# Optimization experiments

Measured on AMD Instinct MI355X. Metric: run time of the kernel, lower is better.

The kernel has to match this reference:

```python
import jax, jax.numpy as jnp
import numpy as np
import math

EPS = 1e-5
GN_GROUPS = 32


def conv2d(x, w, padding):
    # x: [B,C,H,W], w: [O,I,kh,kw]
    return jax.lax.conv_general_dilated(
        x, w, window_strides=(1, 1), padding=[(padding, padding)] * 2,
        dimension_numbers=("NCHW", "OIHW", "NCHW"))


def group_norm(x, weight, bias, groups=GN_GROUPS, eps=EPS):
    B, C, H, W = x.shape
    xg = x.reshape(B, groups, C // groups, H, W)
    mu = xg.mean(axis=(2, 3, 4), keepdims=True)
    var = xg.var(axis=(2, 3, 4), keepdims=True)
    xn = (xg - mu) * jax.lax.rsqrt(var + eps)
    xn = xn.reshape(B, C, H, W)
    return xn * weight[None, :, None, None] + bias[None, :, None, None]


def setup_inputs() -> dict:
    key = jax.random.key(0)
    ks = jax.random.split(key, 8)
    B, C, H, W = 8, 256, 80, 80
    init_gate = 0.99
    gate_bias_val = 0.5 * math.log((1 + init_gate) / (1 - init_gate))
    return {
        "x": jax.random.normal(ks[0], (B, C, H, W), dtype=jnp.float32),
        "w1": jax.random.normal(ks[1], (C, C, 3, 3), dtype=jnp.float32) * 0.01,
        "gn1_w": jnp.ones((C,), dtype=jnp.float32),
        "gn1_b": jnp.zeros((C,), dtype=jnp.float32),
        "w2": jax.random.normal(ks[2], (C, C, 3, 3), dtype=jnp.float32) * 0.01,
        "gn2_w": jnp.ones((C,), dtype=jnp.float32),
        "gn2_b": jnp.zeros((C,), dtype=jnp.float32),
        "gate_w": jax.random.normal(ks[3], (1, C, 1, 1), dtype=jnp.float32) * 0.01,
        "gate_b": jnp.full((1,), gate_bias_val, dtype=jnp.float32),
    }


def reference(x, w1, gn1_w, gn1_b, w2, gn2_w, gn2_b, gate_w, gate_b):
    # shortcut is identity (in_channels == out_channels, stride 1)
    shortcut = x
    # conv1 -> GN -> ReLU
    h = jax.nn.relu(group_norm(conv2d(x, w1, padding=1), gn1_w, gn1_b))
    # conv2 -> GN
    h = group_norm(conv2d(h, w2, padding=1), gn2_w, gn2_b)
    # SpatialGate: 1x1 conv on the original input, ReTanH activation
    g = conv2d(x, gate_w, padding=0) + gate_b[None, :, None, None]  # [B,1,H,W]
    gate = jnp.clip(jnp.tanh(g), 0.0, None)
    # num_groups == 1: encode/decode are identity reshapes; gate broadcasts over C
    out = h * gate
    return jax.nn.relu(out + shortcut)
```

## Files before the change

### kernel.cpp

```cpp
#include <hip/hip_runtime.h>
#include <math.h>

#define NB   8
#define NC   256
#define NH   80
#define NW   80
#define NHW  6400
#define GN_EPS 1e-5f

typedef __bf16 bf16;
typedef bf16 bf16x2 __attribute__((ext_vector_type(2)));
typedef bf16 bf16x4 __attribute__((ext_vector_type(4)));
typedef bf16 bf16x8 __attribute__((ext_vector_type(8)));
typedef float f32x4 __attribute__((ext_vector_type(4)));

typedef __attribute__((address_space(1))) void gvoid;
typedef __attribute__((address_space(3))) void lvoid;
__device__ __forceinline__ void glds16(const void* g, void* l) {
    __builtin_amdgcn_global_load_lds((const gvoid*)g, (lvoid*)l, 16, 0, 0);
}

#define AW_Q 520
#define AW_T 2080
#define AW_BUF 18720

__global__ __launch_bounds__(256) void setup_kernel(
    const float* __restrict__ w1, const float* __restrict__ w2,
    bf16* __restrict__ wA1, bf16* __restrict__ wA2,
    float* __restrict__ stats)
{
    int blk = blockIdx.x, tid = threadIdx.x;
    if (blk == 0) {
        #pragma unroll
        for (int k = 0; k < 8; k++) stats[tid + k * 256] = 0.0f;
        return;
    }
    int rb = blk - 1;
    const float* w = (rb < 2304) ? w1 : w2;
    bf16* wA       = (rb < 2304) ? wA1 : wA2;
    int idx = (rb % 2304) * 256 + tid;
    int c8 = idx & 7;
    int co = (idx >> 3) & 255;
    int qq = (idx >> 11) & 3;
    int tc = idx >> 13;
    int tap = tc % 9, chunk = tc / 9;
    int ci = chunk * 32 + qq * 8 + c8;
    wA[idx] = (bf16)w[(size_t)(co * 256 + ci) * 9 + tap];
}

__global__ __launch_bounds__(256) void prep1_kernel(
    const float* __restrict__ x, bf16* __restrict__ xp,
    const float* __restrict__ gw, float* __restrict__ gpart)
{
    __shared__ float tile[8 * 84];
    int bid = blockIdx.x;
    int row = bid % 80;
    int cib = (bid / 80) & 31;
    int b   = bid / 2560;
    for (int e = threadIdx.x; e < 640; e += 256) {
        int c8 = e / 80, col = e - c8 * 80;
        tile[c8 * 84 + col] = x[((size_t)(b * NC + cib * 8 + c8) * NH + row) * NW + col];
    }
    __syncthreads();
    size_t base = (((size_t)(b * 32 + cib) * 82 + row + 1) * 82) * 8 + 8;
    for (int t = threadIdx.x; t < 320; t += 256) {
        int e = 2 * t, col = e >> 3, c8 = e & 7;
        bf16x2 pk = { (bf16)tile[c8 * 84 + col], (bf16)tile[(c8 + 1) * 84 + col] };
        *(bf16x2*)(xp + base + e) = pk;
    }
    if (threadIdx.x < 80) {
        int col = threadIdx.x;
        float s = 0.0f;
        #pragma unroll
        for (int c8 = 0; c8 < 8; c8++) s = fmaf(tile[c8 * 84 + col], gw[cib * 8 + c8], s);
        gpart[((size_t)cib * NB + b) * NHW + row * 80 + col] = s;
    }
    const uint4 z4 = make_uint4(0u, 0u, 0u, 0u);
    size_t img = ((size_t)(b * 32 + cib)) * 82;
    if (threadIdx.x < 2) {
        int col = threadIdx.x * 81;
        *(uint4*)(xp + ((img + row + 1) * 82 + col) * 8) = z4;
    }
    if (row == 0 || row == 79) {
        int prow = (row == 0) ? 0 : 81;
        for (int u = threadIdx.x; u < 82; u += 256)
            *(uint4*)(xp + ((img + prow) * 82 + u) * 8) = z4;
    }
}

__global__ __launch_bounds__(320, 3) void conv_kernel(
    const bf16* __restrict__ xp, const bf16* __restrict__ wA,
    bf16* __restrict__ y, float* __restrict__ ssum, float* __restrict__ ssq)
{
    __shared__ __align__(16) bf16 Aw[2 * AW_BUF];
    __shared__ float wgs[8], wgq[8];

    int tid  = threadIdx.x;
    int wid  = tid >> 6;
    int lane = tid & 63;
    int n = lane & 15, q = lane >> 4;

    int bid = blockIdx.x;
    int b   = bid >> 6;
    int rem = bid & 63;
    int ct  = rem >> 4;
    int rt  = rem & 15;
    int co0 = ct * 64, h0 = rt * 5;

    if (tid < 8) { wgs[tid] = 0.0f; wgq[tid] = 0.0f; }

    f32x4 acc[4][5];
    #pragma unroll
    for (int i = 0; i < 4; i++)
        #pragma unroll
        for (int j = 0; j < 5; j++) acc[i][j] = (f32x4){0.f, 0.f, 0.f, 0.f};

    for (int p = wid; p < 36; p += 5) {
        int tap = p >> 2, qq = p & 3;
        glds16((const char*)(wA + ((size_t)p * 256 + co0) * 8) + lane * 16,
               (char*)(Aw + tap * AW_T + qq * AW_Q) + lane * 16);
    }

    for (int c = 0; c < 8; c++) {
        __syncthreads();
        if (c + 1 < 8) {
            bf16* dst = Aw + (((c + 1) & 1) ? AW_BUF : 0);
            for (int p = wid; p < 36; p += 5) {
                int tap = p >> 2, qq = p & 3;
                glds16((const char*)(wA + ((size_t)((c + 1) * 36 + p) * 256 + co0) * 8) + lane * 16,
                       (char*)(dst + tap * AW_T + qq * AW_Q) + lane * 16);
            }
        }
        const bf16* awc = Aw + ((c & 1) ? AW_BUF : 0) + q * AW_Q + n * 8;
        const bf16* xq = xp + (((size_t)(b * 32 + c * 4 + q) * 82 + (h0 + wid)) * 82) * 8 + n * 8;

        #pragma unroll
        for (int r = 0; r < 3; r++) {
            bf16x8 L[15];
            #pragma unroll
            for (int nt = 0; nt < 5; nt++)
                #pragma unroll
                for (int s = 0; s < 3; s++)
                    L[nt * 3 + s] = *(const bf16x8*)(xq + (r * 82 + s + nt * 16) * 8);
            #pragma unroll
            for (int s = 0; s < 3; s++) {
                bf16x8 af[4];
                #pragma unroll
                for (int mt = 0; mt < 4; mt++)
                    af[mt] = *(const bf16x8*)(awc + (r * 3 + s) * AW_T + mt * 128);
                #pragma unroll
                for (int mt = 0; mt < 4; mt++)
                    #pragma unroll
                    for (int nt = 0; nt < 5; nt++)
                        acc[mt][nt] = __builtin_amdgcn_mfma_f32_16x16x32_bf16(
                            af[mt], L[nt * 3 + s], acc[mt][nt], 0, 0, 0);
            }
        }
    }

    int h = h0 + wid;
    #pragma unroll
    for (int mt = 0; mt < 4; mt++) {
        float s1 = 0.0f, s2 = 0.0f;
        int co  = co0 + mt * 16 + q * 4;
        int cib = co >> 3, c8 = co & 7;
        #pragma unroll
        for (int nt = 0; nt < 5; nt++) {
            int col = nt * 16 + n;
            bf16x4 pk;
            #pragma unroll
            for (int rg = 0; rg < 4; rg++) {
                float v = acc[mt][nt][rg];
                pk[rg] = (bf16)v;
                s1 += v;
                s2 = fmaf(v, v, s2);
            }
            *(bf16x4*)(y + ((((size_t)(b * 32 + cib) * 80 + h) * 80 + col) * 8 + c8)) = pk;
        }
        #pragma unroll
        for (int off = 1; off < 16; off <<= 1) {
            s1 += __shfl_xor(s1, off, 64);
            s2 += __shfl_xor(s2, off, 64);
        }
        if (n == 0) {
            int gl = mt * 2 + (q >> 1);
            atomicAdd(&wgs[gl], s1);
            atomicAdd(&wgq[gl], s2);
        }
    }
    __syncthreads();
    if (tid < 8) {
        atomicAdd(&ssum[b * 32 + ct * 8 + tid], wgs[tid]);
        atomicAdd(&ssq [b * 32 + ct * 8 + tid], wgq[tid]);
    }
}

__global__ __launch_bounds__(256) void prep2_kernel(
    const bf16* __restrict__ y, bf16* __restrict__ xp,
    const float* __restrict__ s, const float* __restrict__ sq,
    const float* __restrict__ gamma, const float* __restrict__ beta,
    const float* __restrict__ gpart, const float* __restrict__ gb,
    float* __restrict__ gate)
{
    int bid = blockIdx.x;
    if (bid >= 5120) {
        int i = (bid - 5120) * 256 + threadIdx.x;
        float gs = gb[0];
        #pragma unroll 8
        for (int k = 0; k < 32; k++) gs += gpart[(size_t)k * (NB * NHW) + i];
        gate[i] = fmaxf(tanhf(gs), 0.0f);
        return;
    }
    int b = bid / 640; int rem = bid - b * 640;
    int cib = rem / 20; int rq = rem - cib * 20;
    int gidx = b * 32 + cib;
    const float cnt = (float)(8 * NHW);
    float m  = s[gidx] / cnt;
    float vv = sq[gidx] / cnt - m * m;
    float r  = rsqrtf(vv + GN_EPS);
    const bf16* src = y + (size_t)(b * 32 + cib) * 51200 + rq * 2560;
    for (int u = threadIdx.x; u < 1280; u += 256) {
        int e = 2 * u;
        int row = rq * 4 + e / 640;
        int w640 = e % 640;
        int c8 = e & 7;
        int c = cib * 8 + c8;
        float sc0 = r * gamma[c],     sh0 = beta[c]     - m * sc0;
        float sc1 = r * gamma[c + 1], sh1 = beta[c + 1] - m * sc1;
        bf16x2 iv = *(const bf16x2*)(src + e);
        bf16x2 pk = { (bf16)fmaxf(fmaf((float)iv[0], sc0, sh0), 0.0f),
                      (bf16)fmaxf(fmaf((float)iv[1], sc1, sh1), 0.0f) };
        size_t xidx = (((size_t)(b * 32 + cib) * 82 + row + 1) * 82) * 8 + 8 + w640;
        *(bf16x2*)(xp + xidx) = pk;
    }
}

__global__ __launch_bounds__(256) void final_kernel(
    const bf16* __restrict__ y, const float* __restrict__ x,
    const float* __restrict__ gate,
    const float* __restrict__ s, const float* __restrict__ sq,
    const float* __restrict__ gamma, const float* __restrict__ beta,
    float* __restrict__ out)
{
    __shared__ float lds[8 * 324];
    int bid = blockIdx.x;
    int b = bid / 640; int rem = bid - b * 640;
    int cib = rem / 20; int rq = rem - cib * 20;
    int gidx = b * 32 + cib;
    const float cnt = (float)(8 * NHW);
    float m  = s[gidx] / cnt;
    float vv = sq[gidx] / cnt - m * m;
    float r  = rsqrtf(vv + GN_EPS);
    const bf16* src = y + (size_t)(b * 32 + cib) * 51200 + rq * 2560;
    for (int u = threadIdx.x; u < 1280; u += 256) {
        int e = 2 * u;
        int c8 = e & 7;
        int rc = e >> 3;
        int c = cib * 8 + c8;
        float sc0 = r * gamma[c],     sh0 = beta[c]     - m * sc0;
        float sc1 = r * gamma[c + 1], sh1 = beta[c + 1] - m * sc1;
        bf16x2 iv = *(const bf16x2*)(src + e);
        lds[c8 * 324 + rc]       = fmaf((float)iv[0], sc0, sh0);
        lds[(c8 + 1) * 324 + rc] = fmaf((float)iv[1], sc1, sh1);
    }
    __syncthreads();
    const float* gp = gate + b * NHW + rq * 320;
    for (int e2 = threadIdx.x; e2 < 2560; e2 += 256) {
        int c8 = e2 / 320, rc = e2 - c8 * 320;
        int c = cib * 8 + c8;
        size_t oidx = (size_t)(b * NC + c) * NHW + rq * 320 + rc;
        float v = fmaf(lds[c8 * 324 + rc], gp[rc], x[oidx]);
        out[oidx] = fmaxf(v, 0.0f);
    }
}

extern "C" void kernel_launch(void* const* d_in, const int* in_sizes, int n_in,
                              void* d_out, int out_size, void* d_ws, size_t ws_size,
                              hipStream_t stream)
{
    const float* x     = (const float*)d_in[0];
    const float* w1    = (const float*)d_in[1];
    const float* gn1_w = (const float*)d_in[2];
    const float* gn1_b = (const float*)d_in[3];
    const float* w2    = (const float*)d_in[4];
    const float* gn2_w = (const float*)d_in[5];
    const float* gn2_b = (const float*)d_in[6];
    const float* gw    = (const float*)d_in[7];
    const float* gb    = (const float*)d_in[8];

    bf16*  xp    = (bf16*)d_out;
    float* gpart = (float*)((char*)d_out + 27541504);
    float* out   = (float*)d_out;

    char* wsb = (char*)d_ws;
    bf16*  y     = (bf16*)wsb;
    float* gate  = (float*)(wsb + 26214400);
    bf16*  wA1   = (bf16*)(wsb + 26214400 + 204800);
    bf16*  wA2   = wA1 + 589824;
    float* stats = (float*)(wsb + 26214400 + 204800 + 2 * 1179648);
    float* s1  = stats,        * s1q = stats + 256;
    float* s2  = stats + 1024, * s2q = stats + 1280;

    setup_kernel<<<4609, 256, 0, stream>>>(w1, w2, wA1, wA2, stats);
    prep1_kernel<<<20480, 256, 0, stream>>>(x, xp, gw, gpart);
    conv_kernel<<<512, 320, 0, stream>>>(xp, wA1, y, s1, s1q);
    prep2_kernel<<<5320, 256, 0, stream>>>(y, xp, s1, s1q, gn1_w, gn1_b, gpart, gb, gate);
    conv_kernel<<<512, 320, 0, stream>>>(xp, wA2, y, s2, s2q);
    final_kernel<<<5120, 256, 0, stream>>>(y, x, gate, s2, s2q, gn2_w, gn2_b, out);
}
```

Measured before the change: 315.4 us.

## Merge setup and prep kernels, retile conv to 4-row blocks, double-buffer input rows

Folds the weight-reorder/stats-zero kernel into the input prep kernel, removing one launch. The conv kernel now uses 4 waves per block, each covering one output row (640 blocks ordered channel-tile-major), so there are more blocks to spread across CUs. The input fragments for the next filter row are loaded into a second register buffer while the current row feeds the MFMAs, overlapping global loads with compute. The extra register buffer raises register pressure, and the launch bounds now target 2 blocks per SM instead of 3.

Result: faster. 308.2 us (-2.3%).

```diff
diff --git a/kernel.cpp b/kernel.cpp
--- a/kernel.cpp
+++ b/kernel.cpp
@@ -24,52 +24,51 @@
 #define AW_T 2080
 #define AW_BUF 18720
 
-__global__ __launch_bounds__(256) void setup_kernel(
+__global__ __launch_bounds__(256) void prep_kernel(
+    const float* __restrict__ x, bf16* __restrict__ xp,
+    const float* __restrict__ gw, float* __restrict__ gpart,
     const float* __restrict__ w1, const float* __restrict__ w2,
-    bf16* __restrict__ wA1, bf16* __restrict__ wA2,
-    float* __restrict__ stats)
-{
-    int blk = blockIdx.x, tid = threadIdx.x;
-    if (blk == 0) {
-        #pragma unroll
-        for (int k = 0; k < 8; k++) stats[tid + k * 256] = 0.0f;
+    bf16* __restrict__ wA1, bf16* __restrict__ wA2, float* __restrict__ stats)
+{
+    int bid = blockIdx.x;
+    int tid = threadIdx.x;
+    if (bid >= 20480) {
+        int blk = bid - 20480;
+        if (blk == 0) {
+            #pragma unroll
+            for (int k = 0; k < 8; k++) stats[tid + k * 256] = 0.0f;
+            return;
+        }
+        int rb = blk - 1;
+        const float* w = (rb < 2304) ? w1 : w2;
+        bf16* wA       = (rb < 2304) ? wA1 : wA2;
+        int idx = (rb % 2304) * 256 + tid;
+        int c8 = idx & 7;
+        int co = (idx >> 3) & 255;
+        int qq = (idx >> 11) & 3;
+        int tc = idx >> 13;
+        int tap = tc % 9, chunk = tc / 9;
+        int ci = chunk * 32 + qq * 8 + c8;
+        wA[idx] = (bf16)w[(size_t)(co * 256 + ci) * 9 + tap];
         return;
     }
-    int rb = blk - 1;
-    const float* w = (rb < 2304) ? w1 : w2;
-    bf16* wA       = (rb < 2304) ? wA1 : wA2;
-    int idx = (rb % 2304) * 256 + tid;
-    int c8 = idx & 7;
-    int co = (idx >> 3) & 255;
-    int qq = (idx >> 11) & 3;
-    int tc = idx >> 13;
-    int tap = tc % 9, chunk = tc / 9;
-    int ci = chunk * 32 + qq * 8 + c8;
-    wA[idx] = (bf16)w[(size_t)(co * 256 + ci) * 9 + tap];
-}
-
-__global__ __launch_bounds__(256) void prep1_kernel(
-    const float* __restrict__ x, bf16* __restrict__ xp,
-    const float* __restrict__ gw, float* __restrict__ gpart)
-{
     __shared__ float tile[8 * 84];
-    int bid = blockIdx.x;
     int row = bid % 80;
     int cib = (bid / 80) & 31;
     int b   = bid / 2560;
-    for (int e = threadIdx.x; e < 640; e += 256) {
+    for (int e = tid; e < 640; e += 256) {
         int c8 = e / 80, col = e - c8 * 80;
         tile[c8 * 84 + col] = x[((size_t)(b * NC + cib * 8 + c8) * NH + row) * NW + col];
     }
     __syncthreads();
     size_t base = (((size_t)(b * 32 + cib) * 82 + row + 1) * 82) * 8 + 8;
-    for (int t = threadIdx.x; t < 320; t += 256) {
+    for (int t = tid; t < 320; t += 256) {
         int e = 2 * t, col = e >> 3, c8 = e & 7;
         bf16x2 pk = { (bf16)tile[c8 * 84 + col], (bf16)tile[(c8 + 1) * 84 + col] };
         *(bf16x2*)(xp + base + e) = pk;
     }
-    if (threadIdx.x < 80) {
-        int col = threadIdx.x;
+    if (tid < 80) {
+        int col = tid;
         float s = 0.0f;
         #pragma unroll
         for (int c8 = 0; c8 < 8; c8++) s = fmaf(tile[c8 * 84 + col], gw[cib * 8 + c8], s);
@@ -77,18 +76,18 @@
     }
     const uint4 z4 = make_uint4(0u, 0u, 0u, 0u);
     size_t img = ((size_t)(b * 32 + cib)) * 82;
-    if (threadIdx.x < 2) {
-        int col = threadIdx.x * 81;
+    if (tid < 2) {
+        int col = tid * 81;
         *(uint4*)(xp + ((img + row + 1) * 82 + col) * 8) = z4;
     }
     if (row == 0 || row == 79) {
         int prow = (row == 0) ? 0 : 81;
-        for (int u = threadIdx.x; u < 82; u += 256)
+        for (int u = tid; u < 82; u += 256)
             *(uint4*)(xp + ((img + prow) * 82 + u) * 8) = z4;
     }
 }
 
-__global__ __launch_bounds__(320, 3) void conv_kernel(
+__global__ __launch_bounds__(256, 2) void conv_kernel(
     const bf16* __restrict__ xp, const bf16* __restrict__ wA,
     bf16* __restrict__ y, float* __restrict__ ssum, float* __restrict__ ssq)
 {
@@ -101,11 +100,11 @@
     int n = lane & 15, q = lane >> 4;
 
     int bid = blockIdx.x;
-    int b   = bid >> 6;
-    int rem = bid & 63;
-    int ct  = rem >> 4;
-    int rt  = rem & 15;
-    int co0 = ct * 64, h0 = rt * 5;
+    int ct  = bid / 160;
+    int t   = bid - ct * 160;
+    int b   = t / 20;
+    int rt  = t - b * 20;
+    int co0 = ct * 64, h0 = rt * 4;
 
     if (tid < 8) { wgs[tid] = 0.0f; wgq[tid] = 0.0f; }
 
@@ -115,7 +114,7 @@
         #pragma unroll
         for (int j = 0; j < 5; j++) acc[i][j] = (f32x4){0.f, 0.f, 0.f, 0.f};
 
-    for (int p = wid; p < 36; p += 5) {
+    for (int p = wid; p < 36; p += 4) {
         int tap = p >> 2, qq = p & 3;
         glds16((const char*)(wA + ((size_t)p * 256 + co0) * 8) + lane * 16,
                (char*)(Aw + tap * AW_T + qq * AW_Q) + lane * 16);
@@ -125,7 +124,7 @@
         __syncthreads();
         if (c + 1 < 8) {
             bf16* dst = Aw + (((c + 1) & 1) ? AW_BUF : 0);
-            for (int p = wid; p < 36; p += 5) {
+            for (int p = wid; p < 36; p += 4) {
                 int tap = p >> 2, qq = p & 3;
                 glds16((const char*)(wA + ((size_t)((c + 1) * 36 + p) * 256 + co0) * 8) + lane * 16,
                        (char*)(dst + tap * AW_T + qq * AW_Q) + lane * 16);
@@ -134,14 +133,18 @@
         const bf16* awc = Aw + ((c & 1) ? AW_BUF : 0) + q * AW_Q + n * 8;
         const bf16* xq = xp + (((size_t)(b * 32 + c * 4 + q) * 82 + (h0 + wid)) * 82) * 8 + n * 8;
 
+        bf16x8 L[2][15];
+        #pragma unroll
+        for (int k = 0; k < 15; k++)
+            L[0][k] = *(const bf16x8*)(xq + ((k / 3) * 16 + (k % 3)) * 8);
         #pragma unroll
         for (int r = 0; r < 3; r++) {
-            bf16x8 L[15];
-            #pragma unroll
-            for (int nt = 0; nt < 5; nt++)
+            if (r < 2) {
                 #pragma unroll
-                for (int s = 0; s < 3; s++)
-                    L[nt * 3 + s] = *(const bf16x8*)(xq + (r * 82 + s + nt * 16) * 8);
+                for (int k = 0; k < 15; k++)
+                    L[(r + 1) & 1][k] =
+                        *(const bf16x8*)(xq + ((r + 1) * 82 + (k / 3) * 16 + (k % 3)) * 8);
+            }
             #pragma unroll
             for (int s = 0; s < 3; s++) {
                 bf16x8 af[4];
@@ -153,7 +156,7 @@
                     #pragma unroll
                     for (int nt = 0; nt < 5; nt++)
                         acc[mt][nt] = __builtin_amdgcn_mfma_f32_16x16x32_bf16(
-                            af[mt], L[nt * 3 + s], acc[mt][nt], 0, 0, 0);
+                            af[mt], L[r & 1][nt * 3 + s], acc[mt][nt], 0, 0, 0);
             }
         }
     }
@@ -301,10 +304,9 @@
     float* s1  = stats,        * s1q = stats + 256;
     float* s2  = stats + 1024, * s2q = stats + 1280;
 
-    setup_kernel<<<4609, 256, 0, stream>>>(w1, w2, wA1, wA2, stats);
-    prep1_kernel<<<20480, 256, 0, stream>>>(x, xp, gw, gpart);
-    conv_kernel<<<512, 320, 0, stream>>>(xp, wA1, y, s1, s1q);
+    prep_kernel<<<25089, 256, 0, stream>>>(x, xp, gw, gpart, w1, w2, wA1, wA2, stats);
+    conv_kernel<<<640, 256, 0, stream>>>(xp, wA1, y, s1, s1q);
     prep2_kernel<<<5320, 256, 0, stream>>>(y, xp, s1, s1q, gn1_w, gn1_b, gpart, gb, gate);
-    conv_kernel<<<512, 320, 0, stream>>>(xp, wA2, y, s2, s2q);
+    conv_kernel<<<640, 256, 0, stream>>>(xp, wA2, y, s2, s2q);
     final_kernel<<<5120, 256, 0, stream>>>(y, x, gate, s2, s2q, gn2_w, gn2_b, out);
 }
```
